# Kernel optimization log

Measured on AMD Instinct MI355X. Metric: run time of the kernel, lower is better.

The kernel has to match this reference:

```python
import jax, jax.numpy as jnp
import numpy as np

B, S, D_IN, D_OUT = 4, 2048, 4096, 16384


def setup_inputs() -> dict:
    key = jax.random.key(0)
    k1, k2, k3, k4 = jax.random.split(key, 4)
    x = jax.random.normal(k1, (B, S, D_IN), dtype=jnp.float32)
    # per-channel symmetric int8 weights, [out_features, in_features]
    weight_int8 = jax.random.randint(k2, (D_OUT, D_IN), -128, 128, dtype=jnp.int32).astype(jnp.int8)
    # per-channel weight scales (positive, realistic magnitude)
    weight_scale = jax.random.uniform(k3, (D_OUT,), dtype=jnp.float32) * 0.01 + 1e-4
    # static per-tensor activation scale (calibrated constant)
    act_scale = jnp.float32(0.02)
    bias = jax.random.normal(k4, (D_OUT,), dtype=jnp.float32) * 0.1
    return {"x": x, "weight_int8": weight_int8, "weight_scale": weight_scale,
            "act_scale": act_scale, "bias": bias}


def reference(x, weight_int8, weight_scale, act_scale, bias):
    orig_shape = x.shape
    orig_dtype = x.dtype
    x2d = x.reshape(-1, orig_shape[-1])  # [M, D_in]
    # static per-tensor symmetric activation quantization
    x_int8 = jnp.clip(jnp.round(x2d.astype(jnp.float32) / act_scale), -128, 127).astype(jnp.int8)
    y_int32 = jnp.matmul(x_int8, weight_int8.T, preferred_element_type=jnp.int32)  # [M, D_out]
    output_scale = (act_scale * weight_scale).astype(jnp.float32)  # [D_out]
    y = y_int32.astype(jnp.float32) * output_scale[None, :] + bias.astype(jnp.float32)[None, :]
    return y.reshape(*orig_shape[:-1], y.shape[-1]).astype(orig_dtype)
```

## Files before the change

kernel.cpp:

```cpp
#include <hip/hip_runtime.h>
#include <stdint.h>

#define GAS __attribute__((address_space(1)))
#define LAS __attribute__((address_space(3)))

typedef int v4i __attribute__((ext_vector_type(4)));

constexpr int Mdim = 8192;
constexpr int Ndim = 16384;
constexpr int Kdim = 4096;

__device__ __forceinline__ int pack4i8(int a, int b, int c, int d) {
    return (a & 255) | ((b & 255) << 8) | ((c & 255) << 16) | ((d & 255) << 24);
}

__device__ __forceinline__ int qz(float v, float inv) {
    return (int)fminf(fmaxf(rintf(v * inv), -128.0f), 127.0f);
}

__global__ void k_quant_x(const float* __restrict__ x, const float* __restrict__ asc,
                          int8_t* __restrict__ xq) {
    const int i = blockIdx.x * blockDim.x + threadIdx.x;
    const float inv = 1.0f / *asc;
    const float4* xv = (const float4*)x + (size_t)i * 4;
    float4 f0 = xv[0], f1 = xv[1], f2 = xv[2], f3 = xv[3];
    int4 o;
    o.x = pack4i8(qz(f0.x, inv), qz(f0.y, inv), qz(f0.z, inv), qz(f0.w, inv));
    o.y = pack4i8(qz(f1.x, inv), qz(f1.y, inv), qz(f1.z, inv), qz(f1.w, inv));
    o.z = pack4i8(qz(f2.x, inv), qz(f2.y, inv), qz(f2.z, inv), qz(f2.w, inv));
    o.w = pack4i8(qz(f3.x, inv), qz(f3.y, inv), qz(f3.z, inv), qz(f3.w, inv));
    ((int4*)xq)[i] = o;
}

__global__ void k_conv_w(const int* __restrict__ w, int8_t* __restrict__ wq) {
    const int i = blockIdx.x * blockDim.x + threadIdx.x;
    const int4* wv = (const int4*)w + (size_t)i * 4;
    int4 a = wv[0], b = wv[1], c = wv[2], d = wv[3];
    int4 o;
    o.x = pack4i8(a.x, a.y, a.z, a.w);
    o.y = pack4i8(b.x, b.y, b.z, b.w);
    o.z = pack4i8(c.x, c.y, c.z, c.w);
    o.w = pack4i8(d.x, d.y, d.z, d.w);
    ((int4*)wq)[i] = o;
}

constexpr int NT    = Kdim / 128;
constexpr int NITER = NT / 2;

#define VM10 asm volatile("s_waitcnt vmcnt(10)" ::: "memory")
#define VM8  asm volatile("s_waitcnt vmcnt(8)"  ::: "memory")
#define VM4  asm volatile("s_waitcnt vmcnt(4)"  ::: "memory")
#define VM0  asm volatile("s_waitcnt vmcnt(0)"  ::: "memory")

#define PHASE(ABASE, BBASE, READB, AROW, ACC0, STAGE_STMT, VM_STMT)            \
  {                                                                            \
    if (READB) {                                                               \
      _Pragma("unroll") for (int f = 0; f < 4; ++f)                            \
          bfr[f] = *(const v4i*)(lds + (ABASE) + 32768 + browb + f * 1024);    \
    }                                                                          \
    _Pragma("unroll") for (int f = 0; f < 4; ++f)                              \
        afr[f] = *(const v4i*)(lds + (ABASE) + (AROW) + f * 1024);             \
    STAGE_STMT;                                                                \
    VM_STMT;                                                                   \
    __builtin_amdgcn_s_barrier();                                              \
    asm volatile("s_waitcnt lgkmcnt(0)" ::: "memory");                         \
    __builtin_amdgcn_sched_barrier(0);                                         \
    __builtin_amdgcn_s_setprio(1);                                             \
    _Pragma("unroll") for (int fi = 0; fi < 4; ++fi)                           \
        _Pragma("unroll") for (int fj = 0; fj < 4; ++fj)                       \
            acc[(ACC0) + fi][fj] = __builtin_amdgcn_mfma_i32_16x16x64_i8(      \
                afr[fi], bfr[fj], acc[(ACC0) + fi][fj], 0, 0, 0);              \
    __builtin_amdgcn_s_setprio(0);                                             \
    __builtin_amdgcn_s_barrier();                                              \
  }

__global__ __launch_bounds__(512, 2)
void k_gemm256(const int8_t* __restrict__ Aq, const int8_t* __restrict__ Bq,
               const float* __restrict__ wscale, const float* __restrict__ asc,
               const float* __restrict__ bias, float* __restrict__ out) {
    __shared__ __align__(16) int8_t lds[131072];
    const int tid = threadIdx.x, lane = tid & 63, w = tid >> 6;
    const int wm = w >> 2, wn = w & 3;
    const int lrow = lane & 15, kgrp = lane >> 4;

    const int bid = blockIdx.x;
    const int swz = ((bid & 7) << 8) | (bid >> 3);
    const int mt = swz & 31, nt = swz >> 5;
    const int m0 = mt << 8, n0 = nt << 8;

    const int srow = tid >> 2;
    const int scol = (((tid & 3) ^ ((tid >> 3) & 3)) << 4);
    const int8_t* rowA0 = Aq + (size_t)(m0 + srow) * Kdim + scol;
    const int8_t* rowB0 = Bq + (size_t)(n0 + srow) * Kdim + scol;
    const size_t rb1off = (size_t)128 * Kdim;
    const int dstoff = w << 10;

    auto stA = [&](int t, int ks) {
        int8_t* d = lds + ((t & 1) << 16) + (ks << 14) + dstoff;
        const int8_t* s = rowA0 + t * 128 + ks * 64;
        __builtin_amdgcn_global_load_lds((const GAS void*)s, (LAS void*)d, 16, 0, 0);
        __builtin_amdgcn_global_load_lds((const GAS void*)(s + rb1off), (LAS void*)(d + 8192), 16, 0, 0);
    };
    auto stB = [&](int t, int ks) {
        int8_t* d = lds + ((t & 1) << 16) + 32768 + (ks << 14) + dstoff;
        const int8_t* s = rowB0 + t * 128 + ks * 64;
        __builtin_amdgcn_global_load_lds((const GAS void*)s, (LAS void*)d, 16, 0, 0);
        __builtin_amdgcn_global_load_lds((const GAS void*)(s + rb1off), (LAS void*)(d + 8192), 16, 0, 0);
    };

    const int kc = (kgrp ^ ((lrow >> 1) & 3)) << 4;
    const int arow0 = ((wm << 7) + lrow) * 64 + kc;
    const int arow1 = ((wm << 7) + 64 + lrow) * 64 + kc;
    const int browb = ((wn << 6) + lrow) * 64 + kc;

    v4i acc[8][4];
#pragma unroll
    for (int i = 0; i < 8; ++i)
#pragma unroll
        for (int j = 0; j < 4; ++j) acc[i][j] = (v4i){0, 0, 0, 0};

    v4i afr[4], bfr[4];


    stA(0, 0); stA(0, 1); stB(0, 0); stB(0, 1);
    stA(1, 0); stB(1, 0); stB(1, 1);
    VM0;
    __builtin_amdgcn_s_barrier();

    for (int j = 0; j < NITER - 1; ++j) {
        const int t0 = 2 * j, t1 = 2 * j + 1;
        PHASE(0,     0, true,  arow0, 0, stA(t1, 1),     );
        PHASE(0,     0, false, arow1, 4, stB(t0 + 2, 0), VM10);
        PHASE(16384, 0, true,  arow0, 0, stA(t0 + 2, 0), );
        PHASE(16384, 0, false, arow1, 4, stB(t0 + 2, 1), VM10);
        PHASE(65536, 0, true,  arow0, 0, stA(t0 + 2, 1), );
        PHASE(65536, 0, false, arow1, 4, stB(t1 + 2, 0), VM10);
        PHASE(81920, 0, true,  arow0, 0, stA(t1 + 2, 0), );
        PHASE(81920, 0, false, arow1, 4, stB(t1 + 2, 1), VM10);
    }

    {
        PHASE(0,     0, true,  arow0, 0, stA(31, 1), );
        PHASE(0,     0, false, arow1, 4, ,           VM8);
        PHASE(16384, 0, true,  arow0, 0, ,           );
        PHASE(16384, 0, false, arow1, 4, ,           VM4);
        PHASE(65536, 0, true,  arow0, 0, ,           );
        PHASE(65536, 0, false, arow1, 4, ,           VM0);
        PHASE(81920, 0, true,  arow0, 0, ,           );
        PHASE(81920, 0, false, arow1, 4, ,           );
    }

    const float ascale = *asc;
#pragma unroll
    for (int fj = 0; fj < 4; ++fj) {
        const int col = n0 + (wn << 6) + fj * 16 + lrow;
        const float sc = ascale * wscale[col];
        const float bb = bias[col];
#pragma unroll
        for (int mi = 0; mi < 8; ++mi) {
            const int r0 = m0 + (wm << 7) + mi * 16 + (kgrp << 2);
            float* o = out + (size_t)r0 * Ndim + col;
#pragma unroll
            for (int q = 0; q < 4; ++q)
                o[(size_t)q * Ndim] = (float)acc[mi][fj][q] * sc + bb;
        }
    }
}

template <bool AQ, bool BQ>
__global__ __launch_bounds__(256)
void k_gemm(const int8_t* __restrict__ Aq, const float* __restrict__ Xf,
            const int8_t* __restrict__ Bq, const int* __restrict__ W32,
            const float* __restrict__ wscale, const float* __restrict__ asc,
            const float* __restrict__ bias, float* __restrict__ out) {
    constexpr int BM = 128, BN = 128, BK = 64;
    constexpr int KT = Kdim / BK;
    __shared__ __align__(16) int8_t As[2][BM * BK];
    __shared__ __align__(16) int8_t Bs[2][BN * BK];

    const int tid  = threadIdx.x;
    const int lane = tid & 63;
    const int wid  = tid >> 6;
    const int wm = wid >> 1, wn = wid & 1;
    const int lrow = lane & 15, kgrp = lane >> 4;

    const int cpx = gridDim.x >> 3;
    const int swz = ((int)blockIdx.x & 7) * cpx + ((int)blockIdx.x >> 3);
    const int mt = swz & (Mdim / BM - 1);
    const int nt = swz / (Mdim / BM);
    const int m0 = mt * BM, n0 = nt * BN;

    const float ascale = *asc;
    const float inv = 1.0f / ascale;

    v4i acc[4][4];
#pragma unroll
    for (int i = 0; i < 4; ++i)
#pragma unroll
        for (int j = 0; j < 4; ++j) acc[i][j] = (v4i){0, 0, 0, 0};

    auto stage = [&](int buf, int kt) {
        const int k0 = kt * BK;
        if constexpr (AQ) {
            int8_t* ldsp = &As[buf][wid << 10];
            const int8_t* g = Aq + (size_t)(m0 + (tid >> 2)) * Kdim + k0 + ((tid & 3) << 4);
            __builtin_amdgcn_global_load_lds((const GAS void*)g, (LAS void*)ldsp, 16, 0, 0);
            __builtin_amdgcn_global_load_lds((const GAS void*)(g + (size_t)64 * Kdim),
                                             (LAS void*)(ldsp + 4096), 16, 0, 0);
        } else {
            const int row = tid >> 1, cb = (tid & 1) << 5;
            const float4* src = (const float4*)(Xf + (size_t)(m0 + row) * Kdim + k0 + cb);
            int t[8];
#pragma unroll
            for (int j = 0; j < 8; ++j) {
                float4 f = src[j];
                t[j] = pack4i8(qz(f.x, inv), qz(f.y, inv), qz(f.z, inv), qz(f.w, inv));
            }
            int4* dst = (int4*)&As[buf][row * BK + cb];
            dst[0] = make_int4(t[0], t[1], t[2], t[3]);
            dst[1] = make_int4(t[4], t[5], t[6], t[7]);
        }
        if constexpr (BQ) {
            int8_t* ldsp = &Bs[buf][wid << 10];
            const int8_t* g = Bq + (size_t)(n0 + (tid >> 2)) * Kdim + k0 + ((tid & 3) << 4);
            __builtin_amdgcn_global_load_lds((const GAS void*)g, (LAS void*)ldsp, 16, 0, 0);
            __builtin_amdgcn_global_load_lds((const GAS void*)(g + (size_t)64 * Kdim),
                                             (LAS void*)(ldsp + 4096), 16, 0, 0);
        } else {
            const int row = tid >> 1, cb = (tid & 1) << 5;
            const int4* src = (const int4*)(W32 + (size_t)(n0 + row) * Kdim + k0 + cb);
            int t[8];
#pragma unroll
            for (int j = 0; j < 8; ++j) {
                int4 vv = src[j];
                t[j] = pack4i8(vv.x, vv.y, vv.z, vv.w);
            }
            int4* dst = (int4*)&Bs[buf][row * BK + cb];
            dst[0] = make_int4(t[0], t[1], t[2], t[3]);
            dst[1] = make_int4(t[4], t[5], t[6], t[7]);
        }
    };

    stage(0, 0);
    for (int kt = 0; kt < KT; ++kt) {
        const int cur = kt & 1;
        __syncthreads();
        if (kt + 1 < KT) stage(cur ^ 1, kt + 1);

        v4i a[4], b[4];
        const int koff = kgrp << 4;
#pragma unroll
        for (int i = 0; i < 4; ++i) {
            a[i] = *(const v4i*)&As[cur][(wm * 64 + i * 16 + lrow) * BK + koff];
            b[i] = *(const v4i*)&Bs[cur][(wn * 64 + i * 16 + lrow) * BK + koff];
        }
#pragma unroll
        for (int i = 0; i < 4; ++i)
#pragma unroll
            for (int j = 0; j < 4; ++j)
                acc[i][j] = __builtin_amdgcn_mfma_i32_16x16x64_i8(a[i], b[j], acc[i][j], 0, 0, 0);
    }

#pragma unroll
    for (int j = 0; j < 4; ++j) {
        const int col = n0 + wn * 64 + j * 16 + lrow;
        const float sc = ascale * wscale[col];
        const float bb = bias[col];
#pragma unroll
        for (int i = 0; i < 4; ++i) {
            const int r0 = m0 + wm * 64 + i * 16 + (kgrp << 2);
            float* o = out + (size_t)r0 * Ndim + col;
#pragma unroll
            for (int r = 0; r < 4; ++r)
                o[(size_t)r * Ndim] = (float)acc[i][j][r] * sc + bb;
        }
    }
}

extern "C" void kernel_launch(void* const* d_in, const int* in_sizes, int n_in,
                              void* d_out, int out_size, void* d_ws, size_t ws_size,
                              hipStream_t stream) {
    const float* x      = (const float*)d_in[0];
    const int*   w32    = (const int*)d_in[1];
    const float* wscale = (const float*)d_in[2];
    const float* asc    = (const float*)d_in[3];
    const float* bias   = (const float*)d_in[4];
    float* out = (float*)d_out;

    const size_t nx = (size_t)Mdim * Kdim;
    const size_t nw = (size_t)Ndim * Kdim;
    int8_t* xq = (int8_t*)d_ws;
    int8_t* wq = xq + nx;

    const bool haveX = ws_size >= nx;
    const bool haveW = ws_size >= nx + nw;

    if (haveX) k_quant_x<<<(int)(nx / 16 / 256), 256, 0, stream>>>(x, asc, xq);
    if (haveW) k_conv_w<<<(int)(nw / 16 / 256), 256, 0, stream>>>(w32, wq);

    if (haveW) {
        dim3 grid((Mdim / 256) * (Ndim / 256));
        k_gemm256<<<grid, 512, 0, stream>>>(xq, wq, wscale, asc, bias, out);
    } else if (haveX) {
        dim3 grid((Mdim / 128) * (Ndim / 128));
        k_gemm<true, false><<<grid, 256, 0, stream>>>(xq, x, wq, w32, wscale, asc, bias, out);
    } else {
        dim3 grid((Mdim / 128) * (Ndim / 128));
        k_gemm<false, false><<<grid, 256, 0, stream>>>(xq, x, wq, w32, wscale, asc, bias, out);
    }
}
```

Baseline: 830.1 us.

## Prefetch next LDS fragments during MFMA phase and interleave via sched_group_barrier

Restructures the GEMM main loop so each phase issues the MFMAs on fragments already in registers, then loads the next phase's A/B fragments from LDS. sched_group_barrier interleaves those ds_reads with the MFMAs, which hides LDS latency behind matrix math. It also drops the second s_barrier per phase, reorders the prologue staging, and changes the vmcnt waits and stage scheduling to match. The risks are LDS read-after-overwrite races now that a barrier is gone, and higher register pressure from holding prefetched fragments.

```diff
diff --git a/kernel.cpp b/kernel.cpp
--- a/kernel.cpp
+++ b/kernel.cpp
@@ -47,31 +47,42 @@
 constexpr int NT    = Kdim / 128;
 constexpr int NITER = NT / 2;
 
-#define VM10 asm volatile("s_waitcnt vmcnt(10)" ::: "memory")
+#define SGB __builtin_amdgcn_sched_group_barrier
 #define VM8  asm volatile("s_waitcnt vmcnt(8)"  ::: "memory")
 #define VM4  asm volatile("s_waitcnt vmcnt(4)"  ::: "memory")
 #define VM0  asm volatile("s_waitcnt vmcnt(0)"  ::: "memory")
 
-#define PHASE(ABASE, BBASE, READB, AROW, ACC0, STAGE_STMT, VM_STMT)            \
+#define PH(ACC0, DO_PFA, PFA_BASE, PFA_ROW, DO_PFB, PFB_BASE, STAGE_STMT, VM_STMT) \
   {                                                                            \
-    if (READB) {                                                               \
-      _Pragma("unroll") for (int f = 0; f < 4; ++f)                            \
-          bfr[f] = *(const v4i*)(lds + (ABASE) + 32768 + browb + f * 1024);    \
-    }                                                                          \
-    _Pragma("unroll") for (int f = 0; f < 4; ++f)                              \
-        afr[f] = *(const v4i*)(lds + (ABASE) + (AROW) + f * 1024);             \
     STAGE_STMT;                                                                \
     VM_STMT;                                                                   \
     __builtin_amdgcn_s_barrier();                                              \
-    asm volatile("s_waitcnt lgkmcnt(0)" ::: "memory");                         \
     __builtin_amdgcn_sched_barrier(0);                                         \
     __builtin_amdgcn_s_setprio(1);                                             \
-    _Pragma("unroll") for (int fi = 0; fi < 4; ++fi)                           \
-        _Pragma("unroll") for (int fj = 0; fj < 4; ++fj)                       \
-            acc[(ACC0) + fi][fj] = __builtin_amdgcn_mfma_i32_16x16x64_i8(      \
-                afr[fi], bfr[fj], acc[(ACC0) + fi][fj], 0, 0, 0);              \
+    _Pragma("unroll")                                                          \
+    for (int fi = 0; fi < 4; ++fi) {                                           \
+      _Pragma("unroll")                                                        \
+      for (int fj = 0; fj < 4; ++fj)                                           \
+        acc[(ACC0) + fi][fj] = __builtin_amdgcn_mfma_i32_16x16x64_i8(          \
+            a[fi], b[fj], acc[(ACC0) + fi][fj], 0, 0, 0);                      \
+    }                                                                          \
+    if (DO_PFA) {                                                              \
+      _Pragma("unroll")                                                        \
+      for (int f = 0; f < 4; ++f)                                              \
+        a[f] = *(const v4i*)(lds + (PFA_BASE) + (PFA_ROW) + f * 1024);         \
+    }                                                                          \
+    if (DO_PFB) {                                                              \
+      _Pragma("unroll")                                                        \
+      for (int f = 0; f < 4; ++f)                                              \
+        b[f] = *(const v4i*)(lds + (PFB_BASE) + browb + f * 1024);             \
+    }                                                                          \
+    SGB(0x8, 4, 0); SGB(0x100, 1, 0);                                          \
+    SGB(0x8, 4, 0); SGB(0x100, 1, 0);                                          \
+    SGB(0x8, 4, 0); SGB(0x100, 1, 0);                                          \
+    SGB(0x8, 4, 0); SGB(0x100, 1, 0);                                          \
+    if (DO_PFB) { SGB(0x100, 4, 0); }                                          \
     __builtin_amdgcn_s_setprio(0);                                             \
-    __builtin_amdgcn_s_barrier();                                              \
+    __builtin_amdgcn_sched_barrier(0);                                         \
   }
 
 __global__ __launch_bounds__(512, 2)
@@ -119,35 +130,48 @@
 #pragma unroll
         for (int j = 0; j < 4; ++j) acc[i][j] = (v4i){0, 0, 0, 0};
 
-    v4i afr[4], bfr[4];
-
-
-    stA(0, 0); stA(0, 1); stB(0, 0); stB(0, 1);
-    stA(1, 0); stB(1, 0); stB(1, 1);
-    VM0;
+    v4i a[4], b[4];
+
+    stA(0, 0); stB(0, 0); stA(0, 1); stB(0, 1); stA(1, 0); stB(1, 0);
+    VM8;
     __builtin_amdgcn_s_barrier();
+#pragma unroll
+    for (int f = 0; f < 4; ++f)
+        a[f] = *(const v4i*)(lds + arow0 + f * 1024);
+#pragma unroll
+    for (int f = 0; f < 4; ++f)
+        b[f] = *(const v4i*)(lds + 32768 + browb + f * 1024);
 
     for (int j = 0; j < NITER - 1; ++j) {
         const int t0 = 2 * j, t1 = 2 * j + 1;
-        PHASE(0,     0, true,  arow0, 0, stA(t1, 1),     );
-        PHASE(0,     0, false, arow1, 4, stB(t0 + 2, 0), VM10);
-        PHASE(16384, 0, true,  arow0, 0, stA(t0 + 2, 0), );
-        PHASE(16384, 0, false, arow1, 4, stB(t0 + 2, 1), VM10);
-        PHASE(65536, 0, true,  arow0, 0, stA(t0 + 2, 1), );
-        PHASE(65536, 0, false, arow1, 4, stB(t1 + 2, 0), VM10);
-        PHASE(81920, 0, true,  arow0, 0, stA(t1 + 2, 0), );
-        PHASE(81920, 0, false, arow1, 4, stB(t1 + 2, 1), VM10);
+        PH(0, 1, 0,     arow1, 0, 0,      stA(t1, 1),     (void)0);
+        PH(4, 1, 16384, arow0, 1, 49152,  stB(t1, 1),     VM8);
+        PH(0, 1, 16384, arow1, 0, 0,      stA(t0 + 2, 0), (void)0);
+        PH(4, 1, 65536, arow0, 1, 98304,  stB(t0 + 2, 0), VM8);
+        PH(0, 1, 65536, arow1, 0, 0,      stA(t0 + 2, 1), (void)0);
+        PH(4, 1, 81920, arow0, 1, 114688, stB(t0 + 2, 1), VM8);
+        PH(0, 1, 81920, arow1, 0, 0,      stA(t1 + 2, 0), (void)0);
+        PH(4, 1, 0,     arow0, 1, 32768,  stB(t1 + 2, 0), VM8);
     }
 
     {
-        PHASE(0,     0, true,  arow0, 0, stA(31, 1), );
-        PHASE(0,     0, false, arow1, 4, ,           VM8);
-        PHASE(16384, 0, true,  arow0, 0, ,           );
-        PHASE(16384, 0, false, arow1, 4, ,           VM4);
-        PHASE(65536, 0, true,  arow0, 0, ,           );
-        PHASE(65536, 0, false, arow1, 4, ,           VM0);
-        PHASE(81920, 0, true,  arow0, 0, ,           );
-        PHASE(81920, 0, false, arow1, 4, ,           );
+        PH(0, 1, 0,     arow1, 0, 0,      stA(31, 1), (void)0);
+        PH(4, 1, 16384, arow0, 1, 49152,  stB(31, 1), VM8);
+        PH(0, 1, 16384, arow1, 0, 0,      (void)0,    (void)0);
+        PH(4, 1, 65536, arow0, 1, 98304,  (void)0,    VM4);
+        PH(0, 1, 65536, arow1, 0, 0,      (void)0,    (void)0);
+        PH(4, 1, 81920, arow0, 1, 114688, (void)0,    VM0);
+        PH(0, 1, 81920, arow1, 0, 0,      (void)0,    (void)0);
+        __builtin_amdgcn_s_barrier();
+        __builtin_amdgcn_sched_barrier(0);
+        __builtin_amdgcn_s_setprio(1);
+#pragma unroll
+        for (int fi = 0; fi < 4; ++fi)
+#pragma unroll
+            for (int fj = 0; fj < 4; ++fj)
+                acc[4 + fi][fj] = __builtin_amdgcn_mfma_i32_16x16x64_i8(
+                    a[fi], b[fj], acc[4 + fi][fj], 0, 0, 0);
+        __builtin_amdgcn_s_setprio(0);
     }
 
     const float ascale = *asc;
```

Result: slower. 892.3 us (+7.5%).

## Drop the per-phase trailing barrier and rebalance the A/B staging schedule

Applied to the files above, without the earlier changes.

Each compute phase now has one workgroup barrier instead of two. The explicit lgkmcnt(0) wait is gone, so the compiler inserts its own waits before the fragment registers are used. The prefetch order is reworked so every phase issues one B or A tile load and waits with a uniform vmcnt(8), with B stages issued ahead of A. The aim is less barrier stall and a more even spread of global-to-LDS traffic across phases. The risk is a read-after-write race in LDS if a stage overwrites a buffer other waves are still reading, and a possible loss of latency hiding from the new wait depth.

```diff
diff --git a/kernel.cpp b/kernel.cpp
--- a/kernel.cpp
+++ b/kernel.cpp
@@ -47,12 +47,11 @@
 constexpr int NT    = Kdim / 128;
 constexpr int NITER = NT / 2;
 
-#define VM10 asm volatile("s_waitcnt vmcnt(10)" ::: "memory")
 #define VM8  asm volatile("s_waitcnt vmcnt(8)"  ::: "memory")
 #define VM4  asm volatile("s_waitcnt vmcnt(4)"  ::: "memory")
 #define VM0  asm volatile("s_waitcnt vmcnt(0)"  ::: "memory")
 
-#define PHASE(ABASE, BBASE, READB, AROW, ACC0, STAGE_STMT, VM_STMT)            \
+#define PH(ABASE, READB, AROW, ACC0, STAGE_STMT, VM_STMT)                      \
   {                                                                            \
     if (READB) {                                                               \
       _Pragma("unroll") for (int f = 0; f < 4; ++f)                            \
@@ -63,7 +62,6 @@
     STAGE_STMT;                                                                \
     VM_STMT;                                                                   \
     __builtin_amdgcn_s_barrier();                                              \
-    asm volatile("s_waitcnt lgkmcnt(0)" ::: "memory");                         \
     __builtin_amdgcn_sched_barrier(0);                                         \
     __builtin_amdgcn_s_setprio(1);                                             \
     _Pragma("unroll") for (int fi = 0; fi < 4; ++fi)                           \
@@ -71,7 +69,6 @@
             acc[(ACC0) + fi][fj] = __builtin_amdgcn_mfma_i32_16x16x64_i8(      \
                 afr[fi], bfr[fj], acc[(ACC0) + fi][fj], 0, 0, 0);              \
     __builtin_amdgcn_s_setprio(0);                                             \
-    __builtin_amdgcn_s_barrier();                                              \
   }
 
 __global__ __launch_bounds__(512, 2)
@@ -121,33 +118,31 @@
 
     v4i afr[4], bfr[4];
 
-
-    stA(0, 0); stA(0, 1); stB(0, 0); stB(0, 1);
-    stA(1, 0); stB(1, 0); stB(1, 1);
+    stB(0, 0); stA(0, 0); stB(0, 1); stA(0, 1); stB(1, 0); stA(1, 0);
     VM0;
     __builtin_amdgcn_s_barrier();
 
     for (int j = 0; j < NITER - 1; ++j) {
         const int t0 = 2 * j, t1 = 2 * j + 1;
-        PHASE(0,     0, true,  arow0, 0, stA(t1, 1),     );
-        PHASE(0,     0, false, arow1, 4, stB(t0 + 2, 0), VM10);
-        PHASE(16384, 0, true,  arow0, 0, stA(t0 + 2, 0), );
-        PHASE(16384, 0, false, arow1, 4, stB(t0 + 2, 1), VM10);
-        PHASE(65536, 0, true,  arow0, 0, stA(t0 + 2, 1), );
-        PHASE(65536, 0, false, arow1, 4, stB(t1 + 2, 0), VM10);
-        PHASE(81920, 0, true,  arow0, 0, stA(t1 + 2, 0), );
-        PHASE(81920, 0, false, arow1, 4, stB(t1 + 2, 1), VM10);
+        PH(0,     true,  arow0, 0, stB(t1, 1),     VM8)
+        PH(0,     false, arow1, 4, stA(t1, 1),     VM8)
+        PH(16384, true,  arow0, 0, stB(t0 + 2, 0), VM8)
+        PH(16384, false, arow1, 4, stA(t0 + 2, 0), VM8)
+        PH(65536, true,  arow0, 0, stB(t0 + 2, 1), VM8)
+        PH(65536, false, arow1, 4, stA(t0 + 2, 1), VM8)
+        PH(81920, true,  arow0, 0, stB(t1 + 2, 0), VM8)
+        PH(81920, false, arow1, 4, stA(t1 + 2, 0), VM8)
     }
 
     {
-        PHASE(0,     0, true,  arow0, 0, stA(31, 1), );
-        PHASE(0,     0, false, arow1, 4, ,           VM8);
-        PHASE(16384, 0, true,  arow0, 0, ,           );
-        PHASE(16384, 0, false, arow1, 4, ,           VM4);
-        PHASE(65536, 0, true,  arow0, 0, ,           );
-        PHASE(65536, 0, false, arow1, 4, ,           VM0);
-        PHASE(81920, 0, true,  arow0, 0, ,           );
-        PHASE(81920, 0, false, arow1, 4, ,           );
+        PH(0,     true,  arow0, 0, stB(31, 1), VM8)
+        PH(0,     false, arow1, 4, stA(31, 1), VM8)
+        PH(16384, true,  arow0, 0, (void)0,    (void)0)
+        PH(16384, false, arow1, 4, (void)0,    VM4)
+        PH(65536, true,  arow0, 0, (void)0,    (void)0)
+        PH(65536, false, arow1, 4, (void)0,    VM0)
+        PH(81920, true,  arow0, 0, (void)0,    (void)0)
+        PH(81920, false, arow1, 4, (void)0,    (void)0)
     }
 
     const float ascale = *asc;
```

New measurement: 822.6 us. No clear change (-0.9%).
